# Performance work log

Measured on AMD Instinct MI355X. Metric: run time of the kernel, lower is better.

## Reference

```python
import jax, jax.numpy as jnp
import numpy as np


def setup_inputs() -> dict:
    key = jax.random.key(0)
    k = jax.random.split(key, 4)
    B, F, E, U = 4096, 40, 64, 64
    return {
        "x": jax.random.normal(k[0], (B, F, E), dtype=jnp.float32),
        "attention_W": jax.random.normal(k[1], (E, U), dtype=jnp.float32) * (2.0 / (E + U)) ** 0.5,
        "attention_b": jnp.zeros((U,), dtype=jnp.float32),
        "projection_h": jax.random.normal(k[2], (U, 1), dtype=jnp.float32) * (2.0 / (U + 1)) ** 0.5,
        "projection_p": jax.random.normal(k[3], (E, 1), dtype=jnp.float32) * (2.0 / (E + 1)) ** 0.5,
    }


def reference(x, attention_W, attention_b, projection_h, projection_p):
    # x: [B, F, E] stacked field embeddings (original code takes a list of F [B,1,E])
    F = x.shape[1]
    ri, ci = np.triu_indices(F, k=1)  # static pair indices, P = F*(F-1)/2
    inner_product = x[:, ri, :] * x[:, ci, :]            # [B, P, E]
    attention_tmp = jax.nn.relu(
        jnp.einsum('bpe,eu->bpu', inner_product, attention_W) + attention_b
    )                                                    # [B, P, U]
    scores = jnp.einsum('bpu,uo->bpo', attention_tmp, projection_h)  # [B, P, 1]
    attention_weight = jax.nn.softmax(scores, axis=1)    # softmax over pairs
    attention_output = jnp.sum(inner_product * attention_weight, axis=1)  # [B, E]
    # dropout omitted (inference / eval mode)
    afm_out = attention_output @ projection_p            # [B, 1]
    return afm_out
```

## Files before the change

kernel.cpp:

```cpp
#include <hip/hip_runtime.h>
#include <hip/hip_fp16.h>

typedef _Float16 half8v __attribute__((ext_vector_type(8)));
typedef _Float16 half2v __attribute__((ext_vector_type(2)));
typedef float f32x4 __attribute__((ext_vector_type(4)));

__global__ void afm_prep(const float* __restrict__ W, const float* __restrict__ pvec,
                         unsigned char* __restrict__ ws) {
  const int tid = threadIdx.x;
  _Float16* wf = (_Float16*)ws;
  _Float16* pf = (_Float16*)(ws + 8192);
  unsigned int* tbl = (unsigned int*)(ws + 10240);
  for (int idx = tid; idx < 4096; idx += 256) {
    int j = idx & 7, lane = (idx >> 3) & 63, nt = (idx >> 9) & 3, ks = idx >> 11;
    int k = ks * 32 + (lane >> 4) * 8 + j;
    int u = nt * 16 + (lane & 15);
    wf[idx] = (_Float16)W[k * 64 + u];
  }
  for (int idx = tid; idx < 1024; idx += 256) {
    int j = idx & 7, lane = (idx >> 3) & 63, ks = idx >> 9;
    int k = ks * 32 + (lane >> 4) * 8 + j;
    pf[idx] = ((lane & 15) == 0) ? (_Float16)pvec[k] : (_Float16)0.f;
  }
  for (int p = tid; p < 784; p += 256) {
    int pc = p > 779 ? 779 : p;
    int i = 0, rem = pc;
    while (rem >= 39 - i) { rem -= 39 - i; ++i; }
    int j = i + 1 + rem;
    tbl[p] = ((unsigned)(i * 72) << 16) | (unsigned)(j * 72);
  }
}

#define ISSUE_READS(slot, offw)                                                    \
  do {                                                                             \
    const _Float16* xi_ = &xh[((offw) >> 16) + eoff];                              \
    const _Float16* xj_ = &xh[((offw) & 0xffffu) + eoff];                          \
    xia[slot][0] = *(const half8v*)xi_;                                            \
    xia[slot][1] = *(const half8v*)(xi_ + 32);                                     \
    xja[slot][0] = *(const half8v*)xj_;                                            \
    xja[slot][1] = *(const half8v*)(xj_ + 32);                                     \
  } while (0)

__global__ __launch_bounds__(256) void afm_main(
    const float* __restrict__ x, const float* __restrict__ bvec,
    const float* __restrict__ hvec, const unsigned char* __restrict__ ws,
    float* __restrict__ out) {
  __shared__ __align__(16) _Float16 xh[40 * 72];
  __shared__ __align__(16) unsigned int tblu[784];
  __shared__ float scs[784];
  __shared__ float s2s[784];
  __shared__ float red[12];

  const int tid = threadIdx.x;
  const int b = blockIdx.x;
  const int lane = tid & 63;
  const int wid = tid >> 6;
  const int m = lane & 15, kg = lane >> 4;

  const float4* xg = (const float4*)(x + b * 2560);
  float4 v0 = xg[tid];
  float4 v1 = xg[256 + tid];
  float4 v2;
  if (tid < 128) v2 = xg[512 + tid];

  {
    const float4* tg = (const float4*)(ws + 10240);
    float4* ts = (float4*)tblu;
    if (tid < 196) ts[tid] = tg[tid];
  }

  const half8v* wfg = (const half8v*)ws;
  half8v wf[2][4];
#pragma unroll
  for (int ks = 0; ks < 2; ++ks)
#pragma unroll
    for (int nt = 0; nt < 4; ++nt) wf[ks][nt] = wfg[(ks * 4 + nt) * 64 + lane];
  const half8v* pfg = (const half8v*)(ws + 8192);
  half8v pf[2] = {pfg[lane], pfg[64 + lane]};
  f32x4 buv[4], huv[4];
#pragma unroll
  for (int nt = 0; nt < 4; ++nt) {
    buv[nt] = *(const f32x4*)&bvec[nt * 16 + kg * 4];
    huv[nt] = *(const f32x4*)&hvec[nt * 16 + kg * 4];
  }

  {
    int f = tid >> 4, e4 = tid & 15;
    half2v* dst = (half2v*)&xh[f * 72 + e4 * 4];
    dst[0] = __builtin_bit_cast(half2v, __builtin_amdgcn_cvt_pkrtz(v0.x, v0.y));
    dst[1] = __builtin_bit_cast(half2v, __builtin_amdgcn_cvt_pkrtz(v0.z, v0.w));
  }
  {
    int g = 256 + tid;
    int f = g >> 4, e4 = g & 15;
    half2v* dst = (half2v*)&xh[f * 72 + e4 * 4];
    dst[0] = __builtin_bit_cast(half2v, __builtin_amdgcn_cvt_pkrtz(v1.x, v1.y));
    dst[1] = __builtin_bit_cast(half2v, __builtin_amdgcn_cvt_pkrtz(v1.z, v1.w));
  }
  if (tid < 128) {
    int g = 512 + tid;
    int f = g >> 4, e4 = g & 15;
    half2v* dst = (half2v*)&xh[f * 72 + e4 * 4];
    dst[0] = __builtin_bit_cast(half2v, __builtin_amdgcn_cvt_pkrtz(v2.x, v2.y));
    dst[1] = __builtin_bit_cast(half2v, __builtin_amdgcn_cvt_pkrtz(v2.z, v2.w));
  }
  __syncthreads();

  const int eoff = kg * 8;
  const f32x4 zv = (f32x4){0.f, 0.f, 0.f, 0.f};
  unsigned int off[2];
  half8v xia[2][2], xja[2][2];
  off[0] = tblu[16 * wid + m];
  ISSUE_READS(0, off[0]);
  off[1] = tblu[16 * (wid + 4) + m];
#pragma unroll
  for (int i = 0; i < 13; ++i) {
    const int cur = i & 1, nxt = cur ^ 1;
    if (i < 12) ISSUE_READS(nxt, off[nxt]);
    if (i < 11) {
      int tn = wid + 4 * (i + 2);
      tn = tn > 48 ? 48 : tn;
      off[cur] = tblu[16 * tn + m];
    }
    half8v a0 = xia[cur][0] * xja[cur][0];
    half8v a1 = xia[cur][1] * xja[cur][1];
    f32x4 acc[4];
#pragma unroll
    for (int nt = 0; nt < 4; ++nt) {
      acc[nt] = __builtin_amdgcn_mfma_f32_16x16x32_f16(wf[0][nt], a0, buv[nt], 0, 0, 0);
      acc[nt] = __builtin_amdgcn_mfma_f32_16x16x32_f16(wf[1][nt], a1, acc[nt], 0, 0, 0);
    }
    f32x4 accp = __builtin_amdgcn_mfma_f32_16x16x32_f16(pf[0], a0, zv, 0, 0, 0);
    accp = __builtin_amdgcn_mfma_f32_16x16x32_f16(pf[1], a1, accp, 0, 0, 0);

    float sp0 = fmaxf(acc[0][0], 0.f) * huv[0][0];
    float sp1 = fmaxf(acc[1][0], 0.f) * huv[1][0];
    float sp2 = fmaxf(acc[2][0], 0.f) * huv[2][0];
    float sp3 = fmaxf(acc[3][0], 0.f) * huv[3][0];
#pragma unroll
    for (int r = 1; r < 4; ++r) {
      sp0 = fmaf(fmaxf(acc[0][r], 0.f), huv[0][r], sp0);
      sp1 = fmaf(fmaxf(acc[1][r], 0.f), huv[1][r], sp1);
      sp2 = fmaf(fmaxf(acc[2][r], 0.f), huv[2][r], sp2);
      sp3 = fmaf(fmaxf(acc[3][r], 0.f), huv[3][r], sp3);
    }
    float s = (sp0 + sp1) + (sp2 + sp3);
    s += __shfl_xor(s, 16);
    s += __shfl_xor(s, 32);

    int tt = wid + 4 * i;
    tt = tt > 48 ? 48 : tt;
    if (kg == 0) {
      scs[16 * tt + m] = s;
      s2s[16 * tt + m] = accp[0];
    }
  }
  __syncthreads();

  float sv[4];
  float mx = -1e30f;
#pragma unroll
  for (int k2 = 0; k2 < 4; ++k2) {
    int p = tid + k2 * 256;
    if (p < 780) {
      sv[k2] = scs[p];
      mx = fmaxf(mx, sv[k2]);
    } else {
      sv[k2] = -1e30f;
    }
  }
#pragma unroll
  for (int o = 32; o; o >>= 1) mx = fmaxf(mx, __shfl_xor(mx, o));
  if (lane == 0) red[wid] = mx;
  __syncthreads();
  mx = fmaxf(fmaxf(red[0], red[1]), fmaxf(red[2], red[3]));
  float num = 0.f, den = 0.f;
#pragma unroll
  for (int k2 = 0; k2 < 4; ++k2) {
    int p = tid + k2 * 256;
    if (p < 780) {
      float e = __expf(sv[k2] - mx);
      num += e * s2s[p];
      den += e;
    }
  }
#pragma unroll
  for (int o = 32; o; o >>= 1) {
    num += __shfl_xor(num, o);
    den += __shfl_xor(den, o);
  }
  if (lane == 0) { red[4 + wid] = num; red[8 + wid] = den; }
  __syncthreads();
  if (tid == 0)
    out[b] = (red[4] + red[5] + red[6] + red[7]) /
             (red[8] + red[9] + red[10] + red[11]);
}

extern "C" void kernel_launch(void* const* d_in, const int* in_sizes, int n_in,
                              void* d_out, int out_size, void* d_ws, size_t ws_size,
                              hipStream_t stream) {
  const float* x    = (const float*)d_in[0];
  const float* W    = (const float*)d_in[1];
  const float* bvec = (const float*)d_in[2];
  const float* hvec = (const float*)d_in[3];
  const float* pvec = (const float*)d_in[4];
  float* out = (float*)d_out;
  unsigned char* ws = (unsigned char*)d_ws;

  hipLaunchKernelGGL(afm_prep, dim3(1), dim3(256), 0, stream, W, pvec, ws);
  hipLaunchKernelGGL(afm_main, dim3(4096), dim3(256), 0, stream,
                     x, bvec, hvec, ws, out);
}
```

Baseline: 129.7 us.

## Use 512-thread blocks and replace cross-lane score shuffles with LDS partials

Doubles the block to 8 wavefronts so each wave handles about 7 pair tiles instead of 13, shortening the per-block serial MFMA loop and giving more latency hiding per block. The per-pair score reduction across the four k-groups no longer uses two xor shuffles; each lane writes its partial into a 4-wide LDS array that the softmax phase sums when it reads it. The softmax and reductions are rewritten for 8 waves. In exchange, the larger block uses more registers and LDS per block, which may lower how many blocks fit on a CU, and the tail tiles are clamped, so some waves repeat the last tile.

```diff
diff --git a/kernel.cpp b/kernel.cpp
--- a/kernel.cpp
+++ b/kernel.cpp
@@ -41,15 +41,15 @@
     xja[slot][1] = *(const half8v*)(xj_ + 32);                                     \
   } while (0)
 
-__global__ __launch_bounds__(256) void afm_main(
+__global__ __launch_bounds__(512) void afm_main(
     const float* __restrict__ x, const float* __restrict__ bvec,
     const float* __restrict__ hvec, const unsigned char* __restrict__ ws,
     float* __restrict__ out) {
   __shared__ __align__(16) _Float16 xh[40 * 72];
   __shared__ __align__(16) unsigned int tblu[784];
-  __shared__ float scs[784];
+  __shared__ __align__(16) float part[784][4];
   __shared__ float s2s[784];
-  __shared__ float red[12];
+  __shared__ float red[24];
 
   const int tid = threadIdx.x;
   const int b = blockIdx.x;
@@ -59,9 +59,8 @@
 
   const float4* xg = (const float4*)(x + b * 2560);
   float4 v0 = xg[tid];
-  float4 v1 = xg[256 + tid];
-  float4 v2;
-  if (tid < 128) v2 = xg[512 + tid];
+  float4 v1;
+  if (tid < 128) v1 = xg[512 + tid];
 
   {
     const float4* tg = (const float4*)(ws + 10240);
@@ -90,19 +89,12 @@
     dst[0] = __builtin_bit_cast(half2v, __builtin_amdgcn_cvt_pkrtz(v0.x, v0.y));
     dst[1] = __builtin_bit_cast(half2v, __builtin_amdgcn_cvt_pkrtz(v0.z, v0.w));
   }
-  {
-    int g = 256 + tid;
+  if (tid < 128) {
+    int g = 512 + tid;
     int f = g >> 4, e4 = g & 15;
     half2v* dst = (half2v*)&xh[f * 72 + e4 * 4];
     dst[0] = __builtin_bit_cast(half2v, __builtin_amdgcn_cvt_pkrtz(v1.x, v1.y));
     dst[1] = __builtin_bit_cast(half2v, __builtin_amdgcn_cvt_pkrtz(v1.z, v1.w));
-  }
-  if (tid < 128) {
-    int g = 512 + tid;
-    int f = g >> 4, e4 = g & 15;
-    half2v* dst = (half2v*)&xh[f * 72 + e4 * 4];
-    dst[0] = __builtin_bit_cast(half2v, __builtin_amdgcn_cvt_pkrtz(v2.x, v2.y));
-    dst[1] = __builtin_bit_cast(half2v, __builtin_amdgcn_cvt_pkrtz(v2.z, v2.w));
   }
   __syncthreads();
 
@@ -112,13 +104,17 @@
   half8v xia[2][2], xja[2][2];
   off[0] = tblu[16 * wid + m];
   ISSUE_READS(0, off[0]);
-  off[1] = tblu[16 * (wid + 4) + m];
-#pragma unroll
-  for (int i = 0; i < 13; ++i) {
+  {
+    int tn = wid + 8;
+    tn = tn > 48 ? 48 : tn;
+    off[1] = tblu[16 * tn + m];
+  }
+#pragma unroll
+  for (int i = 0; i < 7; ++i) {
     const int cur = i & 1, nxt = cur ^ 1;
-    if (i < 12) ISSUE_READS(nxt, off[nxt]);
-    if (i < 11) {
-      int tn = wid + 4 * (i + 2);
+    if (i < 6) ISSUE_READS(nxt, off[nxt]);
+    if (i < 5) {
+      int tn = wid + 8 * (i + 2);
       tn = tn > 48 ? 48 : tn;
       off[cur] = tblu[16 * tn + m];
     }
@@ -144,56 +140,53 @@
       sp2 = fmaf(fmaxf(acc[2][r], 0.f), huv[2][r], sp2);
       sp3 = fmaf(fmaxf(acc[3][r], 0.f), huv[3][r], sp3);
     }
-    float s = (sp0 + sp1) + (sp2 + sp3);
-    s += __shfl_xor(s, 16);
-    s += __shfl_xor(s, 32);
-
-    int tt = wid + 4 * i;
+    float sp = (sp0 + sp1) + (sp2 + sp3);
+
+    int tt = wid + 8 * i;
     tt = tt > 48 ? 48 : tt;
-    if (kg == 0) {
-      scs[16 * tt + m] = s;
-      s2s[16 * tt + m] = accp[0];
-    }
-  }
-  __syncthreads();
-
-  float sv[4];
-  float mx = -1e30f;
-#pragma unroll
-  for (int k2 = 0; k2 < 4; ++k2) {
-    int p = tid + k2 * 256;
-    if (p < 780) {
-      sv[k2] = scs[p];
-      mx = fmaxf(mx, sv[k2]);
-    } else {
-      sv[k2] = -1e30f;
-    }
-  }
+    part[16 * tt + m][kg] = sp;
+    if (kg == 0) s2s[16 * tt + m] = accp[0];
+  }
+  __syncthreads();
+
+  const f32x4* part4 = (const f32x4*)part;
+  const int p1 = tid + 512;
+  f32x4 q0 = part4[tid];
+  float s0 = (q0[0] + q0[1]) + (q0[2] + q0[3]);
+  float s1 = -1e30f;
+  if (p1 < 780) {
+    f32x4 q1 = part4[p1];
+    s1 = (q1[0] + q1[1]) + (q1[2] + q1[3]);
+  }
+  float mx = fmaxf(s0, s1);
 #pragma unroll
   for (int o = 32; o; o >>= 1) mx = fmaxf(mx, __shfl_xor(mx, o));
   if (lane == 0) red[wid] = mx;
   __syncthreads();
-  mx = fmaxf(fmaxf(red[0], red[1]), fmaxf(red[2], red[3]));
-  float num = 0.f, den = 0.f;
-#pragma unroll
-  for (int k2 = 0; k2 < 4; ++k2) {
-    int p = tid + k2 * 256;
-    if (p < 780) {
-      float e = __expf(sv[k2] - mx);
-      num += e * s2s[p];
-      den += e;
-    }
+  mx = red[0];
+#pragma unroll
+  for (int w = 1; w < 8; ++w) mx = fmaxf(mx, red[w]);
+  float e0 = __expf(s0 - mx);
+  float num = e0 * s2s[tid];
+  float den = e0;
+  if (p1 < 780) {
+    float e1 = __expf(s1 - mx);
+    num += e1 * s2s[p1];
+    den += e1;
   }
 #pragma unroll
   for (int o = 32; o; o >>= 1) {
     num += __shfl_xor(num, o);
     den += __shfl_xor(den, o);
   }
-  if (lane == 0) { red[4 + wid] = num; red[8 + wid] = den; }
-  __syncthreads();
-  if (tid == 0)
-    out[b] = (red[4] + red[5] + red[6] + red[7]) /
-             (red[8] + red[9] + red[10] + red[11]);
+  if (lane == 0) { red[8 + wid] = num; red[16 + wid] = den; }
+  __syncthreads();
+  if (tid == 0) {
+    float ns = 0.f, ds = 0.f;
+#pragma unroll
+    for (int w = 0; w < 8; ++w) { ns += red[8 + w]; ds += red[16 + w]; }
+    out[b] = ns / ds;
+  }
 }
 
 extern "C" void kernel_launch(void* const* d_in, const int* in_sizes, int n_in,
@@ -208,6 +201,6 @@
   unsigned char* ws = (unsigned char*)d_ws;
 
   hipLaunchKernelGGL(afm_prep, dim3(1), dim3(256), 0, stream, W, pvec, ws);
-  hipLaunchKernelGGL(afm_main, dim3(4096), dim3(256), 0, stream,
+  hipLaunchKernelGGL(afm_main, dim3(4096), dim3(512), 0, stream,
                      x, bvec, hvec, ws, out);
 }
```

New measurement: 156.2 us. 20.4% more time.

## Process two batch rows per workgroup to amortize per-block setup

Applied to the files above, without the earlier changes.

Each workgroup now handles two batch samples instead of one, halving the grid to 2048 blocks. Pair-table offsets for the second sample are shifted by a fixed LDS offset, the tile loop runs over 98 tiles instead of 49, and the softmax reduction is done for both samples together. The aim is to spread the per-block weight and register loading, table staging, and barrier cost over twice the work. In exchange LDS use per block roughly doubles and there are fewer blocks in flight, which can reduce occupancy and latency hiding.

```diff
diff --git a/kernel.cpp b/kernel.cpp
--- a/kernel.cpp
+++ b/kernel.cpp
@@ -45,11 +45,11 @@
     const float* __restrict__ x, const float* __restrict__ bvec,
     const float* __restrict__ hvec, const unsigned char* __restrict__ ws,
     float* __restrict__ out) {
-  __shared__ __align__(16) _Float16 xh[40 * 72];
+  __shared__ __align__(16) _Float16 xh[80 * 72];
   __shared__ __align__(16) unsigned int tblu[784];
-  __shared__ float scs[784];
-  __shared__ float s2s[784];
-  __shared__ float red[12];
+  __shared__ float scs[1568];
+  __shared__ float s2s[1568];
+  __shared__ float red[24];
 
   const int tid = threadIdx.x;
   const int b = blockIdx.x;
@@ -57,11 +57,12 @@
   const int wid = tid >> 6;
   const int m = lane & 15, kg = lane >> 4;
 
-  const float4* xg = (const float4*)(x + b * 2560);
+  const float4* xg = (const float4*)(x + b * 5120);
   float4 v0 = xg[tid];
   float4 v1 = xg[256 + tid];
-  float4 v2;
-  if (tid < 128) v2 = xg[512 + tid];
+  float4 v2 = xg[512 + tid];
+  float4 v3 = xg[768 + tid];
+  float4 v4 = xg[1024 + tid];
 
   {
     const float4* tg = (const float4*)(ws + 10240);
@@ -84,26 +85,20 @@
     huv[nt] = *(const f32x4*)&hvec[nt * 16 + kg * 4];
   }
 
-  {
-    int f = tid >> 4, e4 = tid & 15;
-    half2v* dst = (half2v*)&xh[f * 72 + e4 * 4];
-    dst[0] = __builtin_bit_cast(half2v, __builtin_amdgcn_cvt_pkrtz(v0.x, v0.y));
-    dst[1] = __builtin_bit_cast(half2v, __builtin_amdgcn_cvt_pkrtz(v0.z, v0.w));
-  }
-  {
-    int g = 256 + tid;
-    int f = g >> 4, e4 = g & 15;
-    half2v* dst = (half2v*)&xh[f * 72 + e4 * 4];
-    dst[0] = __builtin_bit_cast(half2v, __builtin_amdgcn_cvt_pkrtz(v1.x, v1.y));
-    dst[1] = __builtin_bit_cast(half2v, __builtin_amdgcn_cvt_pkrtz(v1.z, v1.w));
-  }
-  if (tid < 128) {
-    int g = 512 + tid;
-    int f = g >> 4, e4 = g & 15;
-    half2v* dst = (half2v*)&xh[f * 72 + e4 * 4];
-    dst[0] = __builtin_bit_cast(half2v, __builtin_amdgcn_cvt_pkrtz(v2.x, v2.y));
-    dst[1] = __builtin_bit_cast(half2v, __builtin_amdgcn_cvt_pkrtz(v2.z, v2.w));
-  }
+#define STAGE_X(vv, base)                                                          \
+  do {                                                                             \
+    int g = (base) + tid;                                                          \
+    int f = g >> 4, e4 = g & 15;                                                   \
+    half2v* dst = (half2v*)&xh[f * 72 + e4 * 4];                                   \
+    dst[0] = __builtin_bit_cast(half2v, __builtin_amdgcn_cvt_pkrtz((vv).x, (vv).y)); \
+    dst[1] = __builtin_bit_cast(half2v, __builtin_amdgcn_cvt_pkrtz((vv).z, (vv).w)); \
+  } while (0)
+  STAGE_X(v0, 0);
+  STAGE_X(v1, 256);
+  STAGE_X(v2, 512);
+  STAGE_X(v3, 768);
+  STAGE_X(v4, 1024);
+#undef STAGE_X
   __syncthreads();
 
   const int eoff = kg * 8;
@@ -114,13 +109,16 @@
   ISSUE_READS(0, off[0]);
   off[1] = tblu[16 * (wid + 4) + m];
 #pragma unroll
-  for (int i = 0; i < 13; ++i) {
+  for (int i = 0; i < 25; ++i) {
     const int cur = i & 1, nxt = cur ^ 1;
-    if (i < 12) ISSUE_READS(nxt, off[nxt]);
-    if (i < 11) {
+    if (i < 24) ISSUE_READS(nxt, off[nxt]);
+    if (i < 23) {
       int tn = wid + 4 * (i + 2);
-      tn = tn > 48 ? 48 : tn;
-      off[cur] = tblu[16 * tn + m];
+      tn = tn > 97 ? 97 : tn;
+      int bn = tn >= 49;
+      int ttn = tn - (bn ? 49 : 0);
+      unsigned o = tblu[16 * ttn + m];
+      off[cur] = o + (bn ? 0x0B400B40u : 0u);
     }
     half8v a0 = xia[cur][0] * xja[cur][0];
     half8v a1 = xia[cur][1] * xja[cur][1];
@@ -148,52 +146,73 @@
     s += __shfl_xor(s, 16);
     s += __shfl_xor(s, 32);
 
-    int tt = wid + 4 * i;
-    tt = tt > 48 ? 48 : tt;
+    int t = wid + 4 * i;
+    t = t > 97 ? 97 : t;
+    int bt = t >= 49;
+    int tt = t - (bt ? 49 : 0);
     if (kg == 0) {
-      scs[16 * tt + m] = s;
-      s2s[16 * tt + m] = accp[0];
-    }
-  }
-  __syncthreads();
-
-  float sv[4];
-  float mx = -1e30f;
+      int idx = (bt ? 784 : 0) + 16 * tt + m;
+      scs[idx] = s;
+      s2s[idx] = accp[0];
+    }
+  }
+  __syncthreads();
+
+  float sv0[4], sv1[4];
+  float mx0 = -1e30f, mx1 = -1e30f;
 #pragma unroll
   for (int k2 = 0; k2 < 4; ++k2) {
     int p = tid + k2 * 256;
     if (p < 780) {
-      sv[k2] = scs[p];
-      mx = fmaxf(mx, sv[k2]);
+      sv0[k2] = scs[p];
+      sv1[k2] = scs[784 + p];
+      mx0 = fmaxf(mx0, sv0[k2]);
+      mx1 = fmaxf(mx1, sv1[k2]);
     } else {
-      sv[k2] = -1e30f;
-    }
-  }
-#pragma unroll
-  for (int o = 32; o; o >>= 1) mx = fmaxf(mx, __shfl_xor(mx, o));
-  if (lane == 0) red[wid] = mx;
-  __syncthreads();
-  mx = fmaxf(fmaxf(red[0], red[1]), fmaxf(red[2], red[3]));
-  float num = 0.f, den = 0.f;
+      sv0[k2] = -1e30f;
+      sv1[k2] = -1e30f;
+    }
+  }
+#pragma unroll
+  for (int o = 32; o; o >>= 1) {
+    mx0 = fmaxf(mx0, __shfl_xor(mx0, o));
+    mx1 = fmaxf(mx1, __shfl_xor(mx1, o));
+  }
+  if (lane == 0) { red[wid] = mx0; red[4 + wid] = mx1; }
+  __syncthreads();
+  mx0 = fmaxf(fmaxf(red[0], red[1]), fmaxf(red[2], red[3]));
+  mx1 = fmaxf(fmaxf(red[4], red[5]), fmaxf(red[6], red[7]));
+  float num0 = 0.f, den0 = 0.f, num1 = 0.f, den1 = 0.f;
 #pragma unroll
   for (int k2 = 0; k2 < 4; ++k2) {
     int p = tid + k2 * 256;
     if (p < 780) {
-      float e = __expf(sv[k2] - mx);
-      num += e * s2s[p];
-      den += e;
+      float e0 = __expf(sv0[k2] - mx0);
+      num0 += e0 * s2s[p];
+      den0 += e0;
+      float e1 = __expf(sv1[k2] - mx1);
+      num1 += e1 * s2s[784 + p];
+      den1 += e1;
     }
   }
 #pragma unroll
   for (int o = 32; o; o >>= 1) {
-    num += __shfl_xor(num, o);
-    den += __shfl_xor(den, o);
-  }
-  if (lane == 0) { red[4 + wid] = num; red[8 + wid] = den; }
-  __syncthreads();
-  if (tid == 0)
-    out[b] = (red[4] + red[5] + red[6] + red[7]) /
-             (red[8] + red[9] + red[10] + red[11]);
+    num0 += __shfl_xor(num0, o);
+    den0 += __shfl_xor(den0, o);
+    num1 += __shfl_xor(num1, o);
+    den1 += __shfl_xor(den1, o);
+  }
+  if (lane == 0) {
+    red[8 + wid] = num0;  red[12 + wid] = den0;
+    red[16 + wid] = num1; red[20 + wid] = den1;
+  }
+  __syncthreads();
+  if (tid == 0) {
+    out[2 * b] = (red[8] + red[9] + red[10] + red[11]) /
+                 (red[12] + red[13] + red[14] + red[15]);
+    out[2 * b + 1] = (red[16] + red[17] + red[18] + red[19]) /
+                     (red[20] + red[21] + red[22] + red[23]);
+  }
 }
 
 extern "C" void kernel_launch(void* const* d_in, const int* in_sizes, int n_in,
@@ -208,6 +227,6 @@
   unsigned char* ws = (unsigned char*)d_ws;
 
   hipLaunchKernelGGL(afm_prep, dim3(1), dim3(256), 0, stream, W, pvec, ws);
-  hipLaunchKernelGGL(afm_main, dim3(4096), dim3(256), 0, stream,
+  hipLaunchKernelGGL(afm_main, dim3(2048), dim3(256), 0, stream,
                      x, bvec, hvec, ws, out);
 }
```

After: 128.9 us. No clear change (-0.7%).
